# Kernel optimization log

Hardware: AMD Instinct MI355X
Metric: run time of the kernel (lower is better)

The kernel has to match this reference:

```python
import jax, jax.numpy as jnp
import numpy as np

N = 100000
E = 1600000
NEG_SLOPE = 0.2

def _gat_layer(x, src, dst, W, a_s, a_d, b, n):
    # GATConv (heads=1): h = xW; alpha_ij = softmax_i(leaky_relu(a_s.h_j + a_d.h_i))
    h = x @ W                                   # [N, F]
    s_src = h @ a_s                             # [N]
    s_dst = h @ a_d                             # [N]
    logits = jax.nn.leaky_relu(s_src[src] + s_dst[dst], NEG_SLOPE)  # [E]
    m = jax.ops.segment_max(logits, dst, num_segments=n)
    m = jnp.where(jnp.isfinite(m), m, 0.0)
    w = jnp.exp(logits - m[dst])
    denom = jax.ops.segment_sum(w, dst, num_segments=n)
    alpha = w / (denom[dst] + 1e-16)            # neighbor softmax per target node
    out = jax.ops.segment_sum(alpha[:, None] * h[src], dst, num_segments=n)
    return out + b

def setup_inputs() -> dict:
    key = jax.random.key(0)
    ks = jax.random.split(key, 12)
    def glorot(k, shape):
        fan = shape[0] + shape[-1] if len(shape) > 1 else shape[0]
        return jax.random.normal(k, shape, jnp.float32) * jnp.sqrt(2.0 / fan)
    x = jax.random.normal(ks[0], (N, 128), jnp.float32)
    edge_index = jax.random.randint(ks[1], (2, E), 0, N, dtype=jnp.int32)
    return {
        'x': x, 'edge_index': edge_index,
        'W1': glorot(ks[2], (128, 64)), 'a1s': glorot(ks[3], (64,)), 'a1d': glorot(ks[4], (64,)), 'b1': jnp.zeros((64,), jnp.float32),
        'W2': glorot(ks[5], (64, 64)), 'a2s': glorot(ks[6], (64,)), 'a2d': glorot(ks[7], (64,)), 'b2': jnp.zeros((64,), jnp.float32),
        'W3': glorot(ks[8], (64, 32)), 'a3s': glorot(ks[9], (32,)), 'a3d': glorot(ks[10], (32,)), 'b3': jnp.zeros((32,), jnp.float32),
    }

def reference(x, edge_index, W1, a1s, a1d, b1, W2, a2s, a2d, b2, W3, a3s, a3d, b3):
    n = x.shape[0]
    # PyG GATConv adds self-loops by default
    loops = jnp.arange(n, dtype=edge_index.dtype)
    src = jnp.concatenate([edge_index[0], loops])
    dst = jnp.concatenate([edge_index[1], loops])
    h = _gat_layer(x, src, dst, W1, a1s, a1d, b1, n)
    h = jax.nn.relu(h)  # dropout is identity in eval mode
    h = _gat_layer(h, src, dst, W2, a2s, a2d, b2, n)
    h = jax.nn.relu(h)
    h = _gat_layer(h, src, dst, W3, a3s, a3d, b3, n)
    return jax.nn.log_softmax(h, axis=1)
```

## Files before the change

### kernel.cpp

```cpp
#include <hip/hip_runtime.h>
#include <cstddef>
#include <cstdint>

#define NEG_SLOPE 0.2f

__device__ __forceinline__ unsigned short f2bf(float f) {
    unsigned int u = __float_as_uint(f);
    u = (u + 0x7fff + ((u >> 16) & 1)) >> 16;
    return (unsigned short)u;
}
__device__ __forceinline__ float bf_lo(unsigned int u) { return __uint_as_float(u << 16); }
__device__ __forceinline__ float bf_hi(unsigned int u) { return __uint_as_float(u & 0xffff0000u); }

typedef __attribute__((ext_vector_type(8))) short bf16x8;
typedef __attribute__((ext_vector_type(4))) float f32x4;
typedef __attribute__((ext_vector_type(2))) float f32x2;


constexpr int BIN_BLOCKS = 256;
constexpr int MAX_NBK = 1024;

__global__ __launch_bounds__(256) void zero_k(int* __restrict__ p, int n) {
    int i = blockIdx.x * blockDim.x + threadIdx.x;
    if (i < n) p[i] = 0;
}

__global__ __launch_bounds__(256) void bin_hist_k(const int* __restrict__ dst, int E,
                                                  int* __restrict__ btot,
                                                  int* __restrict__ blkoff,
                                                  int nbk, int chunk) {
    __shared__ int hist[MAX_NBK];
    for (int i = threadIdx.x; i < nbk; i += 256) hist[i] = 0;
    __syncthreads();
    const int lo = blockIdx.x * chunk;
    const int hi = min(lo + chunk, E);
    for (int e = lo + threadIdx.x; e < hi; e += 256)
        atomicAdd(&hist[dst[e] >> 7], 1);
    __syncthreads();
    const int B = gridDim.x;
    for (int i = threadIdx.x; i < nbk; i += 256)
        blkoff[i * B + blockIdx.x] = atomicAdd(&btot[i], hist[i]);
}

__global__ __launch_bounds__(256) void scan_small_k(const int* __restrict__ btot,
                                                    int* __restrict__ obk, int nbk) {
    __shared__ int sh[MAX_NBK];
    const int tid = threadIdx.x;
    for (int i = tid; i < nbk; i += 256) sh[i] = btot[i];
    __syncthreads();
    if (tid < 64) {
        int run = 0;
        for (int b0 = 0; b0 < nbk; b0 += 64) {
            const int i = b0 + tid;
            int v = (i < nbk) ? sh[i] : 0;
            int inc = v;
#pragma unroll
            for (int o = 1; o < 64; o <<= 1) {
                int u = __shfl_up(inc, o);
                if (tid >= o) inc += u;
            }
            if (i < nbk) sh[i] = run + inc - v;
            run += __shfl(inc, 63);
        }
        if (tid == 0) obk[nbk] = run;
    }
    __syncthreads();
    for (int i = tid; i < nbk; i += 256) obk[i] = sh[i];
}

__global__ __launch_bounds__(256) void bin_scatter_k(const int* __restrict__ ei, int E,
                                                     const int* __restrict__ obk,
                                                     const int* __restrict__ blkoff,
                                                     int* __restrict__ eb, int nbk,
                                                     int chunk) {
    __shared__ int cur[MAX_NBK];
    __shared__ int off_s[MAX_NBK];
    const int B = gridDim.x;
    for (int i = threadIdx.x; i < nbk; i += 256) {
        cur[i] = 0;
        off_s[i] = obk[i] + blkoff[i * B + blockIdx.x];
    }
    __syncthreads();
    const int lo = blockIdx.x * chunk;
    const int hi = min(lo + chunk, E);
    for (int e = lo + threadIdx.x; e < hi; e += 256) {
        int s = ei[e];
        int d = ei[E + e];
        int b = d >> 7;
        int idx = atomicAdd(&cur[b], 1);
        eb[off_s[b] + idx] = (s << 7) | (d & 127);
    }
}

__global__ __launch_bounds__(256) void bucket_build_k(const int* __restrict__ eb,
                                                      const int* __restrict__ obk,
                                                      int* __restrict__ row_ptr,
                                                      int* __restrict__ col,
                                                      int n, int nbk) {
    __shared__ int c[128];
    __shared__ int rp[128];
    const int b = blockIdx.x;
    const int t = threadIdx.x;
    const int beg = obk[b];
    const int end = obk[b + 1];
    const int bbase = beg + b * 128;
    if (t < 128) c[t] = 1;
    __syncthreads();
    for (int i = beg + t; i < end; i += 256)
        atomicAdd(&c[eb[i] & 127], 1);
    __syncthreads();
    if (t < 64) {
        int v0 = c[2 * t], v1 = c[2 * t + 1];
        int pair = v0 + v1;
        int inc = pair;
        for (int o = 1; o < 64; o <<= 1) {
            int u = __shfl_up(inc, o);
            if (t >= o) inc += u;
        }
        int ex = inc - pair;
        rp[2 * t] = bbase + ex;
        rp[2 * t + 1] = bbase + ex + v0;
    }
    __syncthreads();
    const int node = b * 128 + t;
    if (t < 128 && node < n) {
        row_ptr[node] = rp[t];
        col[rp[t]] = node;
    }
    if (b == 0 && t == 0) row_ptr[n] = obk[nbk] + n;
    __syncthreads();
    if (t < 128) c[t] = 1;
    __syncthreads();
    for (int i = beg + t; i < end; i += 256) {
        int p = eb[i];
        int dl = p & 127;
        int idx = atomicAdd(&c[dl], 1);
        col[rp[dl] + idx] = p >> 7;
    }
}


template <int K, int F>
__launch_bounds__(256)
__global__ void gemm_mfma_k(const float* __restrict__ x, const float* __restrict__ W,
                            const float* __restrict__ a_s, const float* __restrict__ a_d,
                            unsigned short* __restrict__ hb, float2* __restrict__ ssd,
                            int n) {
    constexpr int MT = 64;
    constexpr int KP = K + 8;
    constexpr int NT = F / 16;
    constexpr int KC = K / 32;

    __shared__ unsigned short xb[MT * KP];
    __shared__ unsigned short wb[F * KP];

    const int tid = threadIdx.x;
    const int lane = tid & 63;
    const int wv = tid >> 6;
    const int base = blockIdx.x * MT;

    for (int i = tid; i < MT * K / 4; i += 256) {
        int row = i / (K / 4);
        int c4 = i % (K / 4);
        float4 v = make_float4(0.f, 0.f, 0.f, 0.f);
        if (base + row < n)
            v = *(const float4*)&x[(size_t)(base + row) * K + 4 * c4];
        ushort4 b;
        b.x = f2bf(v.x); b.y = f2bf(v.y); b.z = f2bf(v.z); b.w = f2bf(v.w);
        *(ushort4*)&xb[row * KP + 4 * c4] = b;
    }
    for (int i = tid; i < K * F / 4; i += 256) {
        int nn = i % F;
        int k4 = i / F;
        ushort4 b;
        b.x = f2bf(W[(size_t)(4 * k4 + 0) * F + nn]);
        b.y = f2bf(W[(size_t)(4 * k4 + 1) * F + nn]);
        b.z = f2bf(W[(size_t)(4 * k4 + 2) * F + nn]);
        b.w = f2bf(W[(size_t)(4 * k4 + 3) * F + nn]);
        *(ushort4*)&wb[nn * KP + 4 * k4] = b;
    }
    __syncthreads();

    const int mrow = lane & 15;
    const int quad = lane >> 4;

    f32x4 acc[NT];
#pragma unroll
    for (int t = 0; t < NT; ++t) acc[t] = (f32x4){0.f, 0.f, 0.f, 0.f};

#pragma unroll
    for (int kc = 0; kc < KC; ++kc) {
        const int kof = kc * 32 + quad * 8;
        bf16x8 af = *(const bf16x8*)&xb[(wv * 16 + mrow) * KP + kof];
#pragma unroll
        for (int t = 0; t < NT; ++t) {
            bf16x8 bfr = *(const bf16x8*)&wb[(t * 16 + mrow) * KP + kof];
            acc[t] = __builtin_amdgcn_mfma_f32_16x16x32_bf16(af, bfr, acc[t], 0, 0, 0);
        }
    }

    float as_c[NT], ad_c[NT];
#pragma unroll
    for (int t = 0; t < NT; ++t) { as_c[t] = a_s[t * 16 + mrow]; ad_c[t] = a_d[t * 16 + mrow]; }

#pragma unroll
    for (int r = 0; r < 4; ++r) {
        const int node = base + wv * 16 + quad * 4 + r;
        float ps = 0.f, pd = 0.f;
#pragma unroll
        for (int t = 0; t < NT; ++t) {
            ps = fmaf(acc[t][r], as_c[t], ps);
            pd = fmaf(acc[t][r], ad_c[t], pd);
        }
#pragma unroll
        for (int o = 1; o < 16; o <<= 1) {
            ps += __shfl_xor(ps, o);
            pd += __shfl_xor(pd, o);
        }
        if (node < n) {
#pragma unroll
            for (int t = 0; t < NT; ++t)
                hb[(size_t)node * F + t * 16 + mrow] = f2bf(acc[t][r]);
            if (mrow == 0) ssd[node] = make_float2(ps, pd);
        }
    }
}


template <int K, int F>
__launch_bounds__(512)
__global__ void agg_gemm_k(const int* __restrict__ row_ptr, const int* __restrict__ col,
                           const unsigned short* __restrict__ hbi,
                           const float2* __restrict__ ssdi,
                           const float* __restrict__ bias,
                           const float* __restrict__ W,
                           const float* __restrict__ a_s, const float* __restrict__ a_d,
                           unsigned short* __restrict__ hbo, float2* __restrict__ ssdo,
                           int n) {
    static_assert(K == 64, "agg phase assumes 64 input channels");
    constexpr int S = 8;
    constexpr int MT = 64;
    constexpr int KP = K + 8;
    constexpr int NT = F / 16;
    constexpr int KC = K / 32;

    __shared__ unsigned short xb[MT * KP];
    __shared__ unsigned short wb[F * KP];

    const int tid = threadIdx.x;
    const int lane = tid & 63;
    const int wv = tid >> 6;
    const int base = blockIdx.x * MT;

    for (int i = tid; i < K * F / 4; i += 512) {
        int nn = i % F;
        int k4 = i / F;
        ushort4 b;
        b.x = f2bf(W[(size_t)(4 * k4 + 0) * F + nn]);
        b.y = f2bf(W[(size_t)(4 * k4 + 1) * F + nn]);
        b.z = f2bf(W[(size_t)(4 * k4 + 2) * F + nn]);
        b.w = f2bf(W[(size_t)(4 * k4 + 3) * F + nn]);
        *(ushort4*)&wb[nn * KP + 4 * k4] = b;
    }

    const int ls = lane & (S - 1);
    const int lbase = lane - ls;
    const int nl = tid >> 3;
    const int node = base + nl;

    float val[8] = {0.f, 0.f, 0.f, 0.f, 0.f, 0.f, 0.f, 0.f};
    if (node < n) {
        const int beg = row_ptr[node];
        const int end = row_ptr[node + 1];
        const float2 sn = ssdi[node];
        const float sdv = sn.y;
        float z0 = sn.x + sdv;
        z0 = (z0 > 0.f) ? z0 : NEG_SLOPE * z0;

        float s = 0.f;
        f32x2 acc2[4];
#pragma unroll
        for (int i = 0; i < 4; ++i) acc2[i] = (f32x2){0.f, 0.f};

        const int j0 = beg + ls;
        const bool vld0 = j0 < end;
        int c_cur = vld0 ? col[j0] : 0;
        float w_cur = 0.f;
        if (vld0) {
            float z = ssdi[c_cur].x + sdv;
            z = (z > 0.f) ? z : NEG_SLOPE * z;
            w_cur = __expf(z - z0);
        }

        for (int b0 = beg; b0 < end; b0 += S) {
            const int jn = b0 + S + ls;
            const bool vn = jn < end;
            const int c_next = vn ? col[jn] : 0;

            s += w_cur;
            const unsigned int pk =
                ((unsigned int)f2bf(w_cur) << 17) | (unsigned int)c_cur;

            unsigned int pe[8];
#pragma unroll
            for (int t = 0; t < 8; ++t)
                pe[t] = (unsigned int)__shfl((int)pk, lbase + t);

            uint4 hv[8];
#pragma unroll
            for (int t = 0; t < 8; ++t)
                hv[t] = *(const uint4*)&hbi[(size_t)(pe[t] & 0x1ffffu) * K + 8 * ls];

            __builtin_amdgcn_sched_barrier(0);

            float w_next = 0.f;
            if (vn) {
                float z = ssdi[c_next].x + sdv;
                z = (z > 0.f) ? z : NEG_SLOPE * z;
                w_next = __expf(z - z0);
            }

#pragma unroll
            for (int t = 0; t < 8; ++t) {
                const float wt = __uint_as_float((pe[t] >> 17) << 16);
                f32x2 p;
                p.x = bf_lo(hv[t].x); p.y = bf_hi(hv[t].x); acc2[0] += p * wt;
                p.x = bf_lo(hv[t].y); p.y = bf_hi(hv[t].y); acc2[1] += p * wt;
                p.x = bf_lo(hv[t].z); p.y = bf_hi(hv[t].z); acc2[2] += p * wt;
                p.x = bf_lo(hv[t].w); p.y = bf_hi(hv[t].w); acc2[3] += p * wt;
            }
            c_cur = c_next;
            w_cur = w_next;
        }
#pragma unroll
        for (int o = S / 2; o; o >>= 1) s += __shfl_xor(s, o);
        const float inv = 1.f / (s + 1e-16f);
        val[0] = acc2[0].x; val[1] = acc2[0].y; val[2] = acc2[1].x; val[3] = acc2[1].y;
        val[4] = acc2[2].x; val[5] = acc2[2].y; val[6] = acc2[3].x; val[7] = acc2[3].y;
#pragma unroll
        for (int i = 0; i < 8; ++i)
            val[i] = fmaxf(val[i] * inv + bias[8 * ls + i], 0.f);
    }
    {
        ushort4 p0, p1;
        p0.x = f2bf(val[0]); p0.y = f2bf(val[1]); p0.z = f2bf(val[2]); p0.w = f2bf(val[3]);
        p1.x = f2bf(val[4]); p1.y = f2bf(val[5]); p1.z = f2bf(val[6]); p1.w = f2bf(val[7]);
        *(ushort4*)&xb[nl * KP + 8 * ls] = p0;
        *(ushort4*)&xb[nl * KP + 8 * ls + 4] = p1;
    }

    __syncthreads();

    if (wv < 4) {
        const int mrow = lane & 15;
        const int quad = lane >> 4;

        f32x4 acc[NT];
#pragma unroll
        for (int t = 0; t < NT; ++t) acc[t] = (f32x4){0.f, 0.f, 0.f, 0.f};

#pragma unroll
        for (int kc = 0; kc < KC; ++kc) {
            const int kof = kc * 32 + quad * 8;
            bf16x8 af = *(const bf16x8*)&xb[(wv * 16 + mrow) * KP + kof];
#pragma unroll
            for (int t = 0; t < NT; ++t) {
                bf16x8 bfr = *(const bf16x8*)&wb[(t * 16 + mrow) * KP + kof];
                acc[t] = __builtin_amdgcn_mfma_f32_16x16x32_bf16(af, bfr, acc[t], 0, 0, 0);
            }
        }

        float as_c[NT], ad_c[NT];
#pragma unroll
        for (int t = 0; t < NT; ++t) { as_c[t] = a_s[t * 16 + mrow]; ad_c[t] = a_d[t * 16 + mrow]; }

#pragma unroll
        for (int r = 0; r < 4; ++r) {
            const int node2 = base + wv * 16 + quad * 4 + r;
            float ps = 0.f, pd = 0.f;
#pragma unroll
            for (int t = 0; t < NT; ++t) {
                ps = fmaf(acc[t][r], as_c[t], ps);
                pd = fmaf(acc[t][r], ad_c[t], pd);
            }
#pragma unroll
            for (int o = 1; o < 16; o <<= 1) {
                ps += __shfl_xor(ps, o);
                pd += __shfl_xor(pd, o);
            }
            if (node2 < n) {
#pragma unroll
                for (int t = 0; t < NT; ++t)
                    hbo[(size_t)node2 * F + t * 16 + mrow] = f2bf(acc[t][r]);
                if (mrow == 0) ssdo[node2] = make_float2(ps, pd);
            }
        }
    }
}


template <int F, int S>
__launch_bounds__(256)
__global__ void gat_agg_k(const int* __restrict__ row_ptr, const int* __restrict__ col,
                          const unsigned short* __restrict__ hb,
                          const float2* __restrict__ ssd,
                          const float* __restrict__ bias,
                          float* __restrict__ out, int n) {
    constexpr int NPW = 64 / S;
    constexpr int NL = F / 8;
    constexpr int Q = S / NL;
    constexpr int D = S / Q;
    const int lane = threadIdx.x & 63;
    const int ls   = lane % S;
    const int q    = ls / NL;
    const int cl   = ls % NL;
    const int lbase = lane - ls;
    const int wave = (blockIdx.x * blockDim.x + threadIdx.x) >> 6;
    const int node = wave * NPW + lane / S;
    if (node >= n) return;

    const int beg = row_ptr[node];
    const int end = row_ptr[node + 1];
    const float2 sn = ssd[node];
    const float sdv = sn.y;
    float z0 = sn.x + sdv;
    z0 = (z0 > 0.f) ? z0 : NEG_SLOPE * z0;

    float s = 0.f;
    f32x2 acc2[4];
#pragma unroll
    for (int i = 0; i < 4; ++i) acc2[i] = (f32x2){0.f, 0.f};

    const int j0 = beg + ls;
    const bool vld0 = j0 < end;
    int c_cur = vld0 ? col[j0] : 0;
    float w_cur = 0.f;
    if (vld0) {
        float z = ssd[c_cur].x + sdv;
        z = (z > 0.f) ? z : NEG_SLOPE * z;
        w_cur = __expf(z - z0);
    }

    for (int b0 = beg; b0 < end; b0 += S) {
        const int jn = b0 + S + ls;
        const bool vn = jn < end;
        const int c_next = vn ? col[jn] : 0;

        s += w_cur;
        const unsigned int pk =
            ((unsigned int)f2bf(w_cur) << 17) | (unsigned int)c_cur;

        unsigned int pe[D];
#pragma unroll
        for (int t = 0; t < D; ++t)
            pe[t] = (unsigned int)__shfl((int)pk, lbase + Q * t + q);

        uint4 hv[D];
#pragma unroll
        for (int t = 0; t < D; ++t)
            hv[t] = *(const uint4*)&hb[(size_t)(pe[t] & 0x1ffffu) * F + 8 * cl];

        __builtin_amdgcn_sched_barrier(0);

        float w_next = 0.f;
        if (vn) {
            float z = ssd[c_next].x + sdv;
            z = (z > 0.f) ? z : NEG_SLOPE * z;
            w_next = __expf(z - z0);
        }

#pragma unroll
        for (int t = 0; t < D; ++t) {
            const float wt = __uint_as_float((pe[t] >> 17) << 16);
            f32x2 p;
            p.x = bf_lo(hv[t].x); p.y = bf_hi(hv[t].x); acc2[0] += p * wt;
            p.x = bf_lo(hv[t].y); p.y = bf_hi(hv[t].y); acc2[1] += p * wt;
            p.x = bf_lo(hv[t].z); p.y = bf_hi(hv[t].z); acc2[2] += p * wt;
            p.x = bf_lo(hv[t].w); p.y = bf_hi(hv[t].w); acc2[3] += p * wt;
        }
        c_cur = c_next;
        w_cur = w_next;
    }

#pragma unroll
    for (int o = S / 2; o; o >>= 1) s += __shfl_xor(s, o);
    float val[8] = {acc2[0].x, acc2[0].y, acc2[1].x, acc2[1].y,
                    acc2[2].x, acc2[2].y, acc2[3].x, acc2[3].y};
#pragma unroll
    for (int o = NL; o < S; o <<= 1) {
#pragma unroll
        for (int i = 0; i < 8; ++i) val[i] += __shfl_xor(val[i], o);
    }

    const float inv = 1.f / (s + 1e-16f);
#pragma unroll
    for (int i = 0; i < 8; ++i)
        val[i] = val[i] * inv + bias[8 * cl + i];

    float lm = val[0];
#pragma unroll
    for (int i = 1; i < 8; ++i) lm = fmaxf(lm, val[i]);
#pragma unroll
    for (int o = 1; o < NL; o <<= 1) lm = fmaxf(lm, __shfl_xor(lm, o));
    float ex = 0.f;
#pragma unroll
    for (int i = 0; i < 8; ++i) ex += __expf(val[i] - lm);
#pragma unroll
    for (int o = 1; o < NL; o <<= 1) ex += __shfl_xor(ex, o);
    const float lse = lm + __logf(ex);
#pragma unroll
    for (int i = 0; i < 8; ++i) val[i] -= lse;

    if (q == 0) {
        float4 v0 = make_float4(val[0], val[1], val[2], val[3]);
        float4 v1 = make_float4(val[4], val[5], val[6], val[7]);
        *(float4*)&out[(size_t)node * F + 8 * cl] = v0;
        *(float4*)&out[(size_t)node * F + 8 * cl + 4] = v1;
    }
}


extern "C" void kernel_launch(void* const* d_in, const int* in_sizes, int n_in,
                              void* d_out, int out_size, void* d_ws, size_t ws_size,
                              hipStream_t stream) {
    const float* x  = (const float*)d_in[0];
    const int*   ei = (const int*)d_in[1];
    const float* W1 = (const float*)d_in[2];
    const float* a1s = (const float*)d_in[3];
    const float* a1d = (const float*)d_in[4];
    const float* b1  = (const float*)d_in[5];
    const float* W2 = (const float*)d_in[6];
    const float* a2s = (const float*)d_in[7];
    const float* a2d = (const float*)d_in[8];
    const float* b2  = (const float*)d_in[9];
    const float* W3 = (const float*)d_in[10];
    const float* a3s = (const float*)d_in[11];
    const float* a3d = (const float*)d_in[12];
    const float* b3  = (const float*)d_in[13];

    const int N = in_sizes[0] / 128;
    const int E = in_sizes[1] / 2;
    const int NBK = (N + 127) / 128;
    const int B = BIN_BLOCKS;

    char* wp = (char*)d_ws;
    auto alloc = [&](size_t bytes) -> void* {
        void* p = wp;
        wp += (bytes + 255) & ~(size_t)255;
        return p;
    };
    int* row_ptr = (int*)alloc((size_t)(N + 1) * 4);
    int* col     = (int*)alloc((size_t)(E + N) * 4);
    unsigned short* hb1 = (unsigned short*)alloc((size_t)N * 64 * 2);
    unsigned short* hb2 = (unsigned short*)alloc((size_t)N * 64 * 2);
    unsigned short* hb3 = (unsigned short*)alloc((size_t)N * 32 * 2);
    float2* ssd1 = (float2*)alloc((size_t)N * 8);
    float2* ssd2 = (float2*)alloc((size_t)N * 8);
    float2* ssd3 = (float2*)alloc((size_t)N * 8);
    int* btot   = (int*)alloc((size_t)NBK * 4);
    int* blkoff = (int*)alloc((size_t)NBK * B * 4);
    int* obk    = (int*)alloc((size_t)(NBK + 1) * 4);
    int* eb     = (int*)alloc((size_t)E * 4);

    const int chunk = (E + B - 1) / B;

    zero_k<<<(NBK + 255) / 256, 256, 0, stream>>>(btot, NBK);
    bin_hist_k<<<B, 256, 0, stream>>>(ei + E, E, btot, blkoff, NBK, chunk);
    scan_small_k<<<1, 256, 0, stream>>>(btot, obk, NBK);
    bin_scatter_k<<<B, 256, 0, stream>>>(ei, E, obk, blkoff, eb, NBK, chunk);
    bucket_build_k<<<NBK, 256, 0, stream>>>(eb, obk, row_ptr, col, N, NBK);

    const int GB = (N + 63) / 64;

    gemm_mfma_k<128, 64><<<GB, 256, 0, stream>>>(x, W1, a1s, a1d, hb1, ssd1, N);
    agg_gemm_k<64, 64><<<GB, 512, 0, stream>>>(row_ptr, col, hb1, ssd1, b1,
                                               W2, a2s, a2d, hb2, ssd2, N);
    agg_gemm_k<64, 32><<<GB, 512, 0, stream>>>(row_ptr, col, hb2, ssd2, b2,
                                               W3, a3s, a3d, hb3, ssd3, N);
    gat_agg_k<32, 16><<<(N + 15) / 16, 256, 0, stream>>>(
        row_ptr, col, hb3, ssd3, b3, (float*)d_out, N);
}
```

Before: 279.2 us.

## Sort nodes by degree within 64-node tiles to balance aggregation lanes

Adds a per-tile bitonic sort that orders the 64 nodes of each tile by in-degree and writes a permutation. The aggregation kernels then process nodes in that order, so the nodes sharing a wavefront have similar edge counts and less lane divergence and idle time in the neighbor loops. Results are written back to the original slot in shared memory or to the original node index, so the output is unchanged. It costs one extra small kernel launch and one indirection per node.

```diff
diff --git a/kernel.cpp b/kernel.cpp
--- a/kernel.cpp
+++ b/kernel.cpp
@@ -140,6 +140,28 @@
 }
 
 
+__global__ __launch_bounds__(256) void tile_sort_k(const int* __restrict__ row_ptr,
+                                                   int* __restrict__ perm,
+                                                   int n, int ntiles) {
+    const int wv = threadIdx.x >> 6;
+    const int lane = threadIdx.x & 63;
+    const int tile = blockIdx.x * 4 + wv;
+    if (tile >= ntiles) return;
+    const int node = tile * 64 + lane;
+    const int deg = (node < n) ? (row_ptr[node + 1] - row_ptr[node]) : 0x3fffff;
+    int key = (deg << 6) | lane;
+    for (int k = 2; k <= 64; k <<= 1) {
+        for (int j = k >> 1; j > 0; j >>= 1) {
+            const int pkey = __shfl_xor(key, j);
+            const bool up = ((lane & k) == 0);
+            const bool keep_min = (((lane & j) == 0) == up);
+            key = keep_min ? min(key, pkey) : max(key, pkey);
+        }
+    }
+    perm[tile * 64 + lane] = tile * 64 + (key & 63);
+}
+
+
 template <int K, int F>
 __launch_bounds__(256)
 __global__ void gemm_mfma_k(const float* __restrict__ x, const float* __restrict__ W,
@@ -230,6 +252,7 @@
 template <int K, int F>
 __launch_bounds__(512)
 __global__ void agg_gemm_k(const int* __restrict__ row_ptr, const int* __restrict__ col,
+                           const int* __restrict__ perm,
                            const unsigned short* __restrict__ hbi,
                            const float2* __restrict__ ssdi,
                            const float* __restrict__ bias,
@@ -266,13 +289,14 @@
     const int ls = lane & (S - 1);
     const int lbase = lane - ls;
     const int nl = tid >> 3;
-    const int node = base + nl;
+    const int pnode = perm[base + nl];
+    const int slot = pnode - base;
 
     float val[8] = {0.f, 0.f, 0.f, 0.f, 0.f, 0.f, 0.f, 0.f};
-    if (node < n) {
-        const int beg = row_ptr[node];
-        const int end = row_ptr[node + 1];
-        const float2 sn = ssdi[node];
+    if (pnode < n) {
+        const int beg = row_ptr[pnode];
+        const int end = row_ptr[pnode + 1];
+        const float2 sn = ssdi[pnode];
         const float sdv = sn.y;
         float z0 = sn.x + sdv;
         z0 = (z0 > 0.f) ? z0 : NEG_SLOPE * z0;
@@ -345,8 +369,8 @@
         ushort4 p0, p1;
         p0.x = f2bf(val[0]); p0.y = f2bf(val[1]); p0.z = f2bf(val[2]); p0.w = f2bf(val[3]);
         p1.x = f2bf(val[4]); p1.y = f2bf(val[5]); p1.z = f2bf(val[6]); p1.w = f2bf(val[7]);
-        *(ushort4*)&xb[nl * KP + 8 * ls] = p0;
-        *(ushort4*)&xb[nl * KP + 8 * ls + 4] = p1;
+        *(ushort4*)&xb[slot * KP + 8 * ls] = p0;
+        *(ushort4*)&xb[slot * KP + 8 * ls + 4] = p1;
     }
 
     __syncthreads();
@@ -402,6 +426,7 @@
 template <int F, int S>
 __launch_bounds__(256)
 __global__ void gat_agg_k(const int* __restrict__ row_ptr, const int* __restrict__ col,
+                          const int* __restrict__ perm,
                           const unsigned short* __restrict__ hb,
                           const float2* __restrict__ ssd,
                           const float* __restrict__ bias,
@@ -416,7 +441,7 @@
     const int cl   = ls % NL;
     const int lbase = lane - ls;
     const int wave = (blockIdx.x * blockDim.x + threadIdx.x) >> 6;
-    const int node = wave * NPW + lane / S;
+    const int node = perm[wave * NPW + lane / S];
     if (node >= n) return;
 
     const int beg = row_ptr[node];
@@ -542,6 +567,7 @@
     const int E = in_sizes[1] / 2;
     const int NBK = (N + 127) / 128;
     const int B = BIN_BLOCKS;
+    const int GB = (N + 63) / 64;
 
     char* wp = (char*)d_ws;
     auto alloc = [&](size_t bytes) -> void* {
@@ -551,6 +577,7 @@
     };
     int* row_ptr = (int*)alloc((size_t)(N + 1) * 4);
     int* col     = (int*)alloc((size_t)(E + N) * 4);
+    int* perm    = (int*)alloc((size_t)GB * 64 * 4);
     unsigned short* hb1 = (unsigned short*)alloc((size_t)N * 64 * 2);
     unsigned short* hb2 = (unsigned short*)alloc((size_t)N * 64 * 2);
     unsigned short* hb3 = (unsigned short*)alloc((size_t)N * 32 * 2);
@@ -569,14 +596,13 @@
     scan_small_k<<<1, 256, 0, stream>>>(btot, obk, NBK);
     bin_scatter_k<<<B, 256, 0, stream>>>(ei, E, obk, blkoff, eb, NBK, chunk);
     bucket_build_k<<<NBK, 256, 0, stream>>>(eb, obk, row_ptr, col, N, NBK);
-
-    const int GB = (N + 63) / 64;
+    tile_sort_k<<<(GB + 3) / 4, 256, 0, stream>>>(row_ptr, perm, N, GB);
 
     gemm_mfma_k<128, 64><<<GB, 256, 0, stream>>>(x, W1, a1s, a1d, hb1, ssd1, N);
-    agg_gemm_k<64, 64><<<GB, 512, 0, stream>>>(row_ptr, col, hb1, ssd1, b1,
+    agg_gemm_k<64, 64><<<GB, 512, 0, stream>>>(row_ptr, col, perm, hb1, ssd1, b1,
                                                W2, a2s, a2d, hb2, ssd2, N);
-    agg_gemm_k<64, 32><<<GB, 512, 0, stream>>>(row_ptr, col, hb2, ssd2, b2,
+    agg_gemm_k<64, 32><<<GB, 512, 0, stream>>>(row_ptr, col, perm, hb2, ssd2, b2,
                                                W3, a3s, a3d, hb3, ssd3, N);
     gat_agg_k<32, 16><<<(N + 15) / 16, 256, 0, stream>>>(
-        row_ptr, col, hb3, ssd3, b3, (float*)d_out, N);
-}
+        row_ptr, col, perm, hb3, ssd3, b3, (float*)d_out, N);
+}
```

Result: slower. 289.0 us (+3.5%).
